# Kernel optimization log

Measured on AMD Instinct MI355X. Metric: run time of the kernel, lower is better.

## Reference

```python
import jax, jax.numpy as jnp
import numpy as np

B, S, D, H, N = 8, 1024, 1024, 16, 16  # batch, seq, hidden, heads, num_ns_tokens
HD = D // H


def setup_inputs() -> dict:
    key = jax.random.key(0)
    ks = jax.random.split(key, 8)
    s = 0.02
    return {
        "x": jax.random.normal(ks[0], (B, S, D), jnp.float32),
        "Wq_shared": jax.random.normal(ks[1], (D, D), jnp.float32) * s,
        "Wk_shared": jax.random.normal(ks[2], (D, D), jnp.float32) * s,
        "Wv_shared": jax.random.normal(ks[3], (D, D), jnp.float32) * s,
        "Wq_ded": jax.random.normal(ks[4], (N, D, D), jnp.float32) * s,
        "Wk_ded": jax.random.normal(ks[5], (N, D, D), jnp.float32) * s,
        "Wv_ded": jax.random.normal(ks[6], (N, D, D), jnp.float32) * s,
        "Wo": jax.random.normal(ks[7], (D, D), jnp.float32) * s,
    }


def reference(x, Wq_shared, Wk_shared, Wv_shared, Wq_ded, Wk_ded, Wv_ded, Wo):
    b, s, d = x.shape
    n = Wq_ded.shape[0]

    def proj(Ws, Wd):
        shared = x @ Ws                                   # [b,s,d]
        ded = jnp.einsum('bnd,ndo->bno', x[:, :n], Wd)    # first n tokens use dedicated weights
        return jnp.concatenate([ded, shared[:, n:]], axis=1)

    q = proj(Wq_shared, Wq_ded).reshape(b, s, H, HD)
    k = proj(Wk_shared, Wk_ded).reshape(b, s, H, HD)
    v = proj(Wv_shared, Wv_ded).reshape(b, s, H, HD)

    scores = jnp.einsum('bqhd,bkhd->bhqk', q, k) / jnp.sqrt(jnp.float32(HD))
    causal = jnp.tril(jnp.ones((s, s), dtype=bool))
    scores = jnp.where(causal, scores, jnp.float32(-1e9))
    attn = jax.nn.softmax(scores, axis=-1)
    out = jnp.einsum('bhqk,bkhd->bqhd', attn, v).reshape(b, s, d)
    output = out @ Wo
    return (output, k, v)
```

## Files before the change

kernel.cpp:

```cpp
#include <hip/hip_runtime.h>
#include <cstdint>


typedef unsigned short u16;
typedef __attribute__((ext_vector_type(8)))  __bf16 bf16x8;
typedef __attribute__((ext_vector_type(8)))  u16    u16x8;
typedef __attribute__((ext_vector_type(4)))  float  f32x4;

#define BSD   (8u * 1024u * 1024u)
#define QSCALE 0.18033688011112042f

__device__ __forceinline__ u16 f2bf(float f) {
    unsigned u = __builtin_bit_cast(unsigned, f);
    u += 0x7fffu + ((u >> 16) & 1u);
    return (u16)(u >> 16);
}

__device__ __forceinline__ unsigned pack_bf2(float p0, float p1) {
    return __builtin_amdgcn_perm(__builtin_bit_cast(unsigned, p1),
                                 __builtin_bit_cast(unsigned, p0), 0x07060302u);
}

__device__ __forceinline__ void gl_lds16(const void* g, void* l) {
    __builtin_amdgcn_global_load_lds(
        (const __attribute__((address_space(1))) unsigned*)g,
        (__attribute__((address_space(3))) unsigned*)l, 16, 0, 0);
}

#define FENCE asm volatile("" ::: "memory")
#define WAITV(n) asm volatile("s_waitcnt vmcnt(" #n ")" ::: "memory")

__global__ __launch_bounds__(256) void cvt_fused(
        const float* __restrict__ Wq, const float* __restrict__ Wk,
        const float* __restrict__ Wv, const float* __restrict__ Wo,
        u16* __restrict__ WTcat, u16* __restrict__ WoT,
        const float4* __restrict__ x, u16* __restrict__ xb) {
    __shared__ float t[32][33];
    int z = blockIdx.z;
    if (z < 4) {
        const float* src = (z == 0) ? Wq : (z == 1) ? Wk : (z == 2) ? Wv : Wo;
        u16* dst = (z < 3) ? (WTcat + (size_t)z * 1024 * 1024) : WoT;
        int k0 = blockIdx.x * 32, n0 = blockIdx.y * 32;
        int xx = threadIdx.x & 31, yy = threadIdx.x >> 5;
#pragma unroll
        for (int i = 0; i < 4; ++i)
            t[yy + 8 * i][xx] = src[(size_t)(k0 + yy + 8 * i) * 1024 + n0 + xx];
        __syncthreads();
#pragma unroll
        for (int i = 0; i < 4; ++i)
            dst[(size_t)(n0 + yy + 8 * i) * 1024 + k0 + xx] = f2bf(t[xx][yy + 8 * i]);
    } else {
        int lb = (z - 4) * 1024 + blockIdx.y * 32 + blockIdx.x;
        int i = lb * 256 + threadIdx.x;
        float4 v = x[i];
        ushort4 o;
        o.x = f2bf(v.x); o.y = f2bf(v.y); o.z = f2bf(v.z); o.w = f2bf(v.w);
        ((ushort4*)xb)[i] = o;
    }
}

__global__ __launch_bounds__(512, 2) void gemm_qkv(
        const u16* __restrict__ A, const u16* __restrict__ Bt,
        float* __restrict__ fout, u16* __restrict__ q_attn,
        u16* __restrict__ k_attn) {
    const int K = 1024, NT = 16;
    __shared__ u16 As[3][128 * 64];
    __shared__ u16 Bs[3][256 * 64];
    int tid = threadIdx.x;
    int w = tid >> 6, lane = tid & 63;
    int m0 = blockIdx.y * 128, n0 = blockIdx.x * 256;
    int wm = w & 1, wn = w >> 1;
    int lr = lane & 15, kg = lane >> 4;

    f32x4 acc[4][4] = {};

    auto stageAll = [&](int buf, int t) {
#pragma unroll
        for (int s = 0; s < 2; ++s) {
            int ci = s * 512 + tid;
            int row = ci >> 3, cg = (ci & 7) ^ (row & 7);
            gl_lds16(A + (size_t)(m0 + row) * K + t * 64 + cg * 8, &As[buf][ci * 8]);
        }
#pragma unroll
        for (int s = 0; s < 4; ++s) {
            int ci = s * 512 + tid;
            int row = ci >> 3, cg = (ci & 7) ^ (row & 7);
            gl_lds16(Bt + (size_t)(n0 + row) * K + t * 64 + cg * 8, &Bs[buf][ci * 8]);
        }
    };

    stageAll(0, 0);
    stageAll(1, 1);
    WAITV(6);
    FENCE; __builtin_amdgcn_s_barrier(); FENCE;

    int cur = 0;
    for (int t = 0; t < NT; ++t) {
        int stb = cur + 2; if (stb >= 3) stb -= 3;
        const u16* Ac = As[cur];
        const u16* Bc = Bs[cur];
        {
            bf16x8 af[4], bf[4];
#pragma unroll
            for (int mi = 0; mi < 4; ++mi) {
                int row = wm * 64 + mi * 16 + lr;
                af[mi] = __builtin_bit_cast(bf16x8,
                    *(const u16x8*)&Ac[row * 64 + ((kg ^ (row & 7)) * 8)]);
            }
#pragma unroll
            for (int ni = 0; ni < 4; ++ni) {
                int row = wn * 64 + ni * 16 + lr;
                bf[ni] = __builtin_bit_cast(bf16x8,
                    *(const u16x8*)&Bc[row * 64 + ((kg ^ (row & 7)) * 8)]);
            }
            if (t + 2 < NT) stageAll(stb, t + 2);
            __builtin_amdgcn_s_setprio(1);
#pragma unroll
            for (int mi = 0; mi < 4; ++mi)
#pragma unroll
                for (int ni = 0; ni < 4; ++ni)
                    acc[mi][ni] = __builtin_amdgcn_mfma_f32_16x16x32_bf16(
                        af[mi], bf[ni], acc[mi][ni], 0, 0, 0);
            __builtin_amdgcn_s_setprio(0);
        }
        {
            bf16x8 af[4], bf[4];
#pragma unroll
            for (int mi = 0; mi < 4; ++mi) {
                int row = wm * 64 + mi * 16 + lr;
                af[mi] = __builtin_bit_cast(bf16x8,
                    *(const u16x8*)&Ac[row * 64 + (((4 + kg) ^ (row & 7)) * 8)]);
            }
#pragma unroll
            for (int ni = 0; ni < 4; ++ni) {
                int row = wn * 64 + ni * 16 + lr;
                bf[ni] = __builtin_bit_cast(bf16x8,
                    *(const u16x8*)&Bc[row * 64 + (((4 + kg) ^ (row & 7)) * 8)]);
            }
            __builtin_amdgcn_s_setprio(1);
#pragma unroll
            for (int mi = 0; mi < 4; ++mi)
#pragma unroll
                for (int ni = 0; ni < 4; ++ni)
                    acc[mi][ni] = __builtin_amdgcn_mfma_f32_16x16x32_bf16(
                        af[mi], bf[ni], acc[mi][ni], 0, 0, 0);
            __builtin_amdgcn_s_setprio(0);
        }
        if (t < NT - 1) {
            if (t + 2 < NT) { WAITV(6); }
            else            { WAITV(0); }
            FENCE; __builtin_amdgcn_s_barrier(); FENCE;
        }
        cur = cur + 1; if (cur >= 3) cur -= 3;
    }

    int matId = n0 >> 10;
    int ncol0 = (n0 & 1023) + wn * 64;
#pragma unroll
    for (int am = 0; am < 4; ++am) {
        int mbase = m0 + wm * 64 + am * 16 + kg * 4;
#pragma unroll
        for (int bn = 0; bn < 4; ++bn) {
            int col = ncol0 + bn * 16 + lr;
#pragma unroll
            for (int r = 0; r < 4; ++r) {
                int mm = mbase + r;
                float v = acc[am][bn][r];
                size_t idx = (size_t)mm * 1024 + col;
                if (matId == 0) {
                    q_attn[idx] = f2bf(v * QSCALE);
                } else if (matId == 1) {
                    fout[(size_t)BSD + idx] = v;
                    k_attn[idx] = f2bf(v);
                } else {
                    fout[(size_t)2 * BSD + idx] = v;
                }
            }
        }
    }
}

#define LDfrag(BUF, bufi, row, ks)                                            \
    __builtin_bit_cast(bf16x8, *(const u16x8*)&BUF[bufi]                      \
        [(row) * 64 + ((((ks) * 4 + kg) ^ ((row) & 7)) * 8)])

#define PH(bufi, mh, nh, STAGE_STMT, GATE_STMT) do {                          \
    bf16x8 af_[2][2], bq_[2][2];                                              \
    _Pragma("unroll") for (int mi = 0; mi < 2; ++mi) {                        \
        int arow = wm * 64 + (mh) * 32 + mi * 16 + lr;                        \
        _Pragma("unroll") for (int ks = 0; ks < 2; ++ks)                      \
            af_[mi][ks] = LDfrag(As, bufi, arow, ks);                         \
    }                                                                         \
    _Pragma("unroll") for (int ni = 0; ni < 2; ++ni) {                        \
        int brow = wn * 64 + (nh) * 32 + ni * 16 + lr;                        \
        _Pragma("unroll") for (int ks = 0; ks < 2; ++ks)                      \
            bq_[ni][ks] = LDfrag(Bs, bufi, brow, ks);                         \
    }                                                                         \
    STAGE_STMT;                                                               \
    GATE_STMT;                                                                \
    FENCE; __builtin_amdgcn_s_barrier(); FENCE;                               \
    asm volatile("s_waitcnt lgkmcnt(0)" ::: "memory");                        \
    __builtin_amdgcn_s_setprio(1);                                            \
    _Pragma("unroll") for (int ks = 0; ks < 2; ++ks)                          \
    _Pragma("unroll") for (int mi = 0; mi < 2; ++mi)                          \
    _Pragma("unroll") for (int ni = 0; ni < 2; ++ni)                          \
        acc[(mh) * 2 + mi][(nh) * 2 + ni] =                                   \
            __builtin_amdgcn_mfma_f32_16x16x32_bf16(                          \
                af_[mi][ks], bq_[ni][ks],                                     \
                acc[(mh) * 2 + mi][(nh) * 2 + ni], 0, 0, 0);                  \
    __builtin_amdgcn_s_setprio(0);                                            \
    FENCE; __builtin_amdgcn_s_barrier(); FENCE;                               \
} while (0)

__global__ __launch_bounds__(512, 2) void gemm8p_wo(
        const u16* __restrict__ A, const u16* __restrict__ Bt,
        float* __restrict__ fout) {
    const int K = 1024, nt = 16;
    __shared__ u16 As[2][128 * 64];
    __shared__ u16 Bs[2][256 * 64];
    int tid = threadIdx.x;
    int w = tid >> 6, lane = tid & 63;
    int m0 = blockIdx.y * 128, n0 = blockIdx.x * 256;
    int wm = w & 1, wn = w >> 1;
    int lr = lane & 15, kg = lane >> 4;

    f32x4 acc[4][4] = {};

    auto stageA = [&](int buf, int half, int t) {
        int ci = ((w & 3) << 6) + lane + ((w >> 2) << 9) + (half << 8);
        int row = ci >> 3, cg = (ci & 7) ^ (row & 7);
        gl_lds16(A + (size_t)(m0 + row) * K + t * 64 + cg * 8, &As[buf][ci * 8]);
    };
    auto stageB = [&](int buf, int half, int t) {
#pragma unroll
        for (int j = 0; j < 2; ++j) {
            int u = w + 8 * j;
            int ci = ((u >> 2) << 9) + ((u & 3) << 6) + lane + (half << 8);
            int row = ci >> 3, cg = (ci & 7) ^ (row & 7);
            gl_lds16(Bt + (size_t)(n0 + row) * K + t * 64 + cg * 8, &Bs[buf][ci * 8]);
        }
    };

    stageA(0, 0, 0);
    stageB(0, 0, 0);
    stageA(0, 1, 0);
    stageB(0, 1, 0);
    WAITV(3);
    FENCE; __builtin_amdgcn_s_barrier(); FENCE;

    for (int t = 0; t < nt - 1; ++t) {
        int cur = t & 1, nxt = cur ^ 1;
        PH(cur, 0, 0, stageA(nxt, 0, t + 1), WAITV(3));
        PH(cur, 1, 0, stageB(nxt, 0, t + 1), WAITV(3));
        PH(cur, 1, 1, stageA(nxt, 1, t + 1), ((void)0));
        PH(cur, 0, 1, stageB(nxt, 1, t + 1), WAITV(3));
    }
    PH(1, 0, 0, ((void)0), WAITV(2));
    PH(1, 1, 0, ((void)0), WAITV(0));
    PH(1, 1, 1, ((void)0), ((void)0));
    PH(1, 0, 1, ((void)0), ((void)0));

#pragma unroll
    for (int am = 0; am < 4; ++am) {
        int mbase = m0 + wm * 64 + am * 16 + kg * 4;
#pragma unroll
        for (int bn = 0; bn < 4; ++bn) {
            int col = n0 + wn * 64 + bn * 16 + lr;
#pragma unroll
            for (int r = 0; r < 4; ++r)
                fout[(size_t)(mbase + r) * 1024 + col] = acc[am][bn][r];
        }
    }
}

__global__ __launch_bounds__(512) void ded_partial(
        const float* __restrict__ x, const float* __restrict__ Wq,
        const float* __restrict__ Wk, const float* __restrict__ Wv,
        float* __restrict__ part) {
    int dc = blockIdx.x, n = blockIdx.y, mat = blockIdx.z;
    const float* W = ((mat == 0) ? Wq : (mat == 1) ? Wk : Wv) +
                     (size_t)n * 1024 * 1024;
    __shared__ float xs[8 * 128];
    __shared__ float4 red[8 * 256];
    int tid = threadIdx.x;
    for (int i = tid; i < 1024; i += 512) {
        int b = i >> 7, d = i & 127;
        xs[i] = x[((size_t)b * 1024 + n) * 1024 + dc * 128 + d];
    }
    __syncthreads();
    int h = tid >> 8, c = tid & 255;
    int o0 = c * 4;
    int dbase = dc * 128 + h * 64;
    float4 acc[8];
#pragma unroll
    for (int b = 0; b < 8; ++b) acc[b] = make_float4(0.f, 0.f, 0.f, 0.f);
    for (int d0 = 0; d0 < 64; d0 += 8) {
        float4 w[8];
#pragma unroll
        for (int j = 0; j < 8; ++j)
            w[j] = *(const float4*)&W[(size_t)(dbase + d0 + j) * 1024 + o0];
#pragma unroll
        for (int j = 0; j < 8; ++j) {
#pragma unroll
            for (int b = 0; b < 8; ++b) {
                float xv = xs[b * 128 + h * 64 + d0 + j];
                acc[b].x += xv * w[j].x;
                acc[b].y += xv * w[j].y;
                acc[b].z += xv * w[j].z;
                acc[b].w += xv * w[j].w;
            }
        }
    }
    if (h == 1) {
#pragma unroll
        for (int b = 0; b < 8; ++b) red[b * 256 + c] = acc[b];
    }
    __syncthreads();
    if (h == 0) {
#pragma unroll
        for (int b = 0; b < 8; ++b) {
            float4 r = red[b * 256 + c];
            acc[b].x += r.x; acc[b].y += r.y; acc[b].z += r.z; acc[b].w += r.w;
            *(float4*)&part[(size_t)(((mat * 8 + dc) * 8 + b) * 16 + n) * 1024 + o0] = acc[b];
        }
    }
}

__global__ __launch_bounds__(256) void fix_vt(
        const float* __restrict__ part, float* __restrict__ d_out,
        u16* __restrict__ q_attn, u16* __restrict__ k_attn,
        const float* __restrict__ vf, u16* __restrict__ vT) {
    __shared__ float t[64][65];
    int bid = blockIdx.x;
    int tid = threadIdx.x;

    if (bid < 384) {
        int mat = bid >> 7, b = (bid >> 4) & 7, n = bid & 15;
        int o0 = tid * 4;
        float v[4] = {0.f, 0.f, 0.f, 0.f};
        for (int dc = 0; dc < 8; ++dc) {
            float4 p = *(const float4*)&part[(size_t)(((mat * 8 + dc) * 8 + b) * 16 + n) * 1024 + o0];
            v[0] += p.x; v[1] += p.y; v[2] += p.z; v[3] += p.w;
        }
#pragma unroll
        for (int j = 0; j < 4; ++j) {
            int col = o0 + j;
            size_t idx = ((size_t)b * 1024 + n) * 1024 + col;
            if (mat == 0) {
                q_attn[idx] = f2bf(v[j] * QSCALE);
            } else if (mat == 1) {
                d_out[(size_t)BSD + idx] = v[j];
                k_attn[idx] = f2bf(v[j]);
            } else {
                d_out[(size_t)2 * BSD + idx] = v[j];
                int h = col >> 6, hd = col & 63;
                vT[((size_t)((b * 16 + h) * 64 + hd)) * 1024 + n] = f2bf(v[j]);
            }
        }
        return;
    }

    int id = bid - 384;
    int st = id & 15, h = (id >> 4) & 15, b = id >> 8;
    int cg = tid & 15, sl = tid >> 4;
#pragma unroll
    for (int p = 0; p < 4; ++p) {
        int s = p * 16 + sl;
        float4 v = *(const float4*)&vf[
            ((size_t)(b * 1024 + st * 64 + s)) * 1024 + h * 64 + cg * 4];
        t[cg * 4 + 0][s] = v.x;
        t[cg * 4 + 1][s] = v.y;
        t[cg * 4 + 2][s] = v.z;
        t[cg * 4 + 3][s] = v.w;
    }
    __syncthreads();
    int hd = tid >> 2, sc = (tid & 3) * 16;
    if (st == 0 && sc == 0) return;
    u16* dst = vT + ((size_t)((b * 16 + h) * 64 + hd)) * 1024 + st * 64 + sc;
#pragma unroll
    for (int c = 0; c < 4; ++c) {
        ushort4 o;
        o.x = f2bf(t[hd][sc + c * 4 + 0]);
        o.y = f2bf(t[hd][sc + c * 4 + 1]);
        o.z = f2bf(t[hd][sc + c * 4 + 2]);
        o.w = f2bf(t[hd][sc + c * 4 + 3]);
        *(ushort4*)(dst + c * 4) = o;
    }
}

__global__ __launch_bounds__(256) void attn(
        const u16* __restrict__ q_attn, const u16* __restrict__ k_attn,
        const u16* __restrict__ vT, u16* __restrict__ O) {
    int qt = 7 - blockIdx.x;
    int h = blockIdx.y, b = blockIdx.z;
    const u16* Qg = q_attn + ((size_t)(b * 1024) + qt * 128) * 1024 + h * 64;
    const u16* Kg = k_attn + ((size_t)(b * 1024)) * 1024 + h * 64;
    const u16* Vg = vT + (size_t)((b * 16 + h) * 64) * 1024;

    __shared__ u16 Qs[128 * 64];
    __shared__ u16 Ks[64 * 64];
    __shared__ u16 Vs[64 * 64];
    __shared__ u16 Ps[128 * 64];
    __shared__ float red[4 * 32];

    int tid = threadIdx.x, wave = tid >> 6, lane = tid & 63;
    int lr = lane & 15, kg = lane >> 4;

#pragma unroll
    for (int j = 0; j < 4; ++j) {
        int ci = j * 256 + tid;
        int row = ci >> 3, cg = (ci & 7) ^ (row & 7);
        gl_lds16(Qg + (size_t)row * 1024 + cg * 8, Qs + ci * 8);
    }

    float l_acc[2] = {0.f, 0.f};
    f32x4 oacc[2][4] = {};

    int nkt = 2 * qt + 2;
    for (int kt = 0; kt < nkt; ++kt) {
        __syncthreads();
#pragma unroll
        for (int j = 0; j < 2; ++j) {
            int ci = j * 256 + tid;
            int row = ci >> 3, cg = (ci & 7) ^ (row & 7);
            gl_lds16(Kg + (size_t)(kt * 64 + row) * 1024 + cg * 8, Ks + ci * 8);
            gl_lds16(Vg + (size_t)row * 1024 + kt * 64 + cg * 8, Vs + ci * 8);
        }
        __syncthreads();

        bool wactive = (qt * 128 + wave * 32 + 31) >= kt * 64;
        if (wactive) {
            f32x4 sacc[4][2] = {};
#pragma unroll
            for (int ks = 0; ks < 2; ++ks) {
                bf16x8 af[4], bq[2];
#pragma unroll
                for (int mi = 0; mi < 4; ++mi) {
                    int row = mi * 16 + lr;
                    af[mi] = __builtin_bit_cast(bf16x8,
                        *(const u16x8*)&Ks[row * 64 + (((ks * 4 + kg) ^ (row & 7)) * 8)]);
                }
#pragma unroll
                for (int nj = 0; nj < 2; ++nj) {
                    int qr = wave * 32 + nj * 16 + lr;
                    bq[nj] = __builtin_bit_cast(bf16x8,
                        *(const u16x8*)&Qs[qr * 64 + (((ks * 4 + kg) ^ (qr & 7)) * 8)]);
                }
#pragma unroll
                for (int mi = 0; mi < 4; ++mi)
#pragma unroll
                    for (int nj = 0; nj < 2; ++nj)
                        sacc[mi][nj] = __builtin_amdgcn_mfma_f32_16x16x32_bf16(
                            af[mi], bq[nj], sacc[mi][nj], 0, 0, 0);
            }

            if (kt >= 2 * qt) {
#pragma unroll
                for (int mi = 0; mi < 4; ++mi)
#pragma unroll
                    for (int nj = 0; nj < 2; ++nj)
#pragma unroll
                        for (int r = 0; r < 4; ++r) {
                            int kk_g = kt * 64 + mi * 16 + kg * 4 + r;
                            int q_g  = qt * 128 + wave * 32 + nj * 16 + lr;
                            if (kk_g > q_g) sacc[mi][nj][r] = -1e30f;
                        }
            }

#pragma unroll
            for (int nj = 0; nj < 2; ++nj) {
                int q = wave * 32 + nj * 16 + lr;
                float lsum = 0.f;
#pragma unroll
                for (int mi = 0; mi < 4; ++mi) {
                    float p0 = __builtin_amdgcn_exp2f(sacc[mi][nj][0]);
                    float p1 = __builtin_amdgcn_exp2f(sacc[mi][nj][1]);
                    float p2 = __builtin_amdgcn_exp2f(sacc[mi][nj][2]);
                    float p3 = __builtin_amdgcn_exp2f(sacc[mi][nj][3]);
                    lsum += (p0 + p1) + (p2 + p3);
                    int kkc = mi * 2 + (kg >> 1);
                    int off = q * 64 + ((kkc ^ (q & 7)) * 8) + (kg & 1) * 4;
                    uint2 w2;
                    w2.x = pack_bf2(p0, p1);
                    w2.y = pack_bf2(p2, p3);
                    *(uint2*)&Ps[off] = w2;
                }
                l_acc[nj] += lsum;
            }

#pragma unroll
            for (int ks = 0; ks < 2; ++ks) {
                bf16x8 ap[2], bv[4];
#pragma unroll
                for (int mi = 0; mi < 2; ++mi) {
                    int q = wave * 32 + mi * 16 + lr;
                    ap[mi] = __builtin_bit_cast(bf16x8,
                        *(const u16x8*)&Ps[q * 64 + (((ks * 4 + kg) ^ (q & 7)) * 8)]);
                }
#pragma unroll
                for (int nj = 0; nj < 4; ++nj) {
                    int hd = nj * 16 + lr;
                    bv[nj] = __builtin_bit_cast(bf16x8,
                        *(const u16x8*)&Vs[hd * 64 + (((ks * 4 + kg) ^ (hd & 7)) * 8)]);
                }
#pragma unroll
                for (int mi = 0; mi < 2; ++mi)
#pragma unroll
                    for (int nj = 0; nj < 4; ++nj)
                        oacc[mi][nj] = __builtin_amdgcn_mfma_f32_16x16x32_bf16(
                            ap[mi], bv[nj], oacc[mi][nj], 0, 0, 0);
            }
        }
    }

#pragma unroll
    for (int nj = 0; nj < 2; ++nj) {
        float l = l_acc[nj];
        l += __shfl_xor(l, 16);
        l += __shfl_xor(l, 32);
        if (kg == 0) red[wave * 32 + nj * 16 + lr] = l;
    }
#pragma unroll
    for (int mi = 0; mi < 2; ++mi) {
        f32x4 lv = *(f32x4*)&red[wave * 32 + mi * 16 + kg * 4];
        f32x4 rv;
#pragma unroll
        for (int r = 0; r < 4; ++r) rv[r] = __builtin_amdgcn_rcpf(lv[r]);
#pragma unroll
        for (int nj = 0; nj < 4; ++nj)
#pragma unroll
            for (int r = 0; r < 4; ++r) {
                int q_local = wave * 32 + mi * 16 + kg * 4 + r;
                size_t row = (size_t)b * 1024 + qt * 128 + q_local;
                O[row * 1024 + h * 64 + nj * 16 + lr] =
                    f2bf(oacc[mi][nj][r] * rv[r]);
            }
    }
}

extern "C" void kernel_launch(void* const* d_in, const int* in_sizes, int n_in,
                              void* d_out, int out_size, void* d_ws, size_t ws_size,
                              hipStream_t stream) {
    const float* x   = (const float*)d_in[0];
    const float* Wq  = (const float*)d_in[1];
    const float* Wk  = (const float*)d_in[2];
    const float* Wv  = (const float*)d_in[3];
    const float* Wqd = (const float*)d_in[4];
    const float* Wkd = (const float*)d_in[5];
    const float* Wvd = (const float*)d_in[6];
    const float* Wo  = (const float*)d_in[7];
    float* out = (float*)d_out;

    char* ws = (char*)d_ws;
    u16*   WTcat  = (u16*)(ws);
    u16*   WoT    = (u16*)(ws + 6291456);
    u16*   xb     = (u16*)(ws + 8388608);
    u16*   q_attn = (u16*)(ws + 25165824);
    u16*   k_attn = (u16*)(ws + 41943040);
    u16*   vT     = (u16*)(ws + 58720256);
    u16*   Ow     = (u16*)(ws + 75497472);
    float* part   = (float*)(ws + 92274688);

    cvt_fused<<<dim3(32, 32, 12), 256, 0, stream>>>(
        Wq, Wk, Wv, Wo, WTcat, WoT, (const float4*)x, xb);
    gemm_qkv<<<dim3(12, 64), 512, 0, stream>>>(xb, WTcat, out, q_attn, k_attn);
    ded_partial<<<dim3(8, 16, 3), 512, 0, stream>>>(x, Wqd, Wkd, Wvd, part);
    fix_vt<<<dim3(2432), 256, 0, stream>>>(
        part, out, q_attn, k_attn, out + (size_t)2 * BSD, vT);
    attn<<<dim3(8, 16, 8), 256, 0, stream>>>(q_attn, k_attn, vT, Ow);
    gemm8p_wo<<<dim3(4, 64), 512, 0, stream>>>(Ow, WoT, out);
}
```

Before: 458.1 us.

## Double-buffer K/V tiles in attention and keep Q fragments in registers

The attention kernel now double-buffers the K and V tiles in LDS. It issues the async global-to-LDS load for the next key tile before computing the current one, and needs only one barrier per iteration instead of two. The Q fragments are loaded once directly from global memory into registers, which removes the Q LDS tile and the repeated LDS reads of Q. Separately, ded_partial gets a launch-bounds occupancy hint of 2 and a partial unroll of its inner loop. The changes trade more LDS for the K/V buffers and more register pressure for better overlap of loads with MFMA work.

```diff
diff --git a/kernel.cpp b/kernel.cpp
--- a/kernel.cpp
+++ b/kernel.cpp
@@ -273,7 +273,7 @@
     }
 }
 
-__global__ __launch_bounds__(512) void ded_partial(
+__global__ __launch_bounds__(512, 2) void ded_partial(
         const float* __restrict__ x, const float* __restrict__ Wq,
         const float* __restrict__ Wk, const float* __restrict__ Wv,
         float* __restrict__ part) {
@@ -294,6 +294,7 @@
     float4 acc[8];
 #pragma unroll
     for (int b = 0; b < 8; ++b) acc[b] = make_float4(0.f, 0.f, 0.f, 0.f);
+#pragma unroll 2
     for (int d0 = 0; d0 < 64; d0 += 8) {
         float4 w[8];
 #pragma unroll
@@ -397,61 +398,63 @@
     const u16* Kg = k_attn + ((size_t)(b * 1024)) * 1024 + h * 64;
     const u16* Vg = vT + (size_t)((b * 16 + h) * 64) * 1024;
 
-    __shared__ u16 Qs[128 * 64];
-    __shared__ u16 Ks[64 * 64];
-    __shared__ u16 Vs[64 * 64];
+    __shared__ u16 Ks[2][64 * 64];
+    __shared__ u16 Vs[2][64 * 64];
     __shared__ u16 Ps[128 * 64];
     __shared__ float red[4 * 32];
 
     int tid = threadIdx.x, wave = tid >> 6, lane = tid & 63;
     int lr = lane & 15, kg = lane >> 4;
 
-#pragma unroll
-    for (int j = 0; j < 4; ++j) {
-        int ci = j * 256 + tid;
-        int row = ci >> 3, cg = (ci & 7) ^ (row & 7);
-        gl_lds16(Qg + (size_t)row * 1024 + cg * 8, Qs + ci * 8);
-    }
-
-    float l_acc[2] = {0.f, 0.f};
-    f32x4 oacc[2][4] = {};
-
-    int nkt = 2 * qt + 2;
-    for (int kt = 0; kt < nkt; ++kt) {
-        __syncthreads();
+    bf16x8 bq_reg[2][2];
+#pragma unroll
+    for (int ks = 0; ks < 2; ++ks)
+#pragma unroll
+        for (int nj = 0; nj < 2; ++nj) {
+            int qr = wave * 32 + nj * 16 + lr;
+            bq_reg[ks][nj] = __builtin_bit_cast(bf16x8,
+                *(const u16x8*)(Qg + (size_t)qr * 1024 + (ks * 4 + kg) * 8));
+        }
+
+    auto stageKV = [&](int buf, int kt) {
 #pragma unroll
         for (int j = 0; j < 2; ++j) {
             int ci = j * 256 + tid;
             int row = ci >> 3, cg = (ci & 7) ^ (row & 7);
-            gl_lds16(Kg + (size_t)(kt * 64 + row) * 1024 + cg * 8, Ks + ci * 8);
-            gl_lds16(Vg + (size_t)row * 1024 + kt * 64 + cg * 8, Vs + ci * 8);
-        }
-        __syncthreads();
+            gl_lds16(Kg + (size_t)(kt * 64 + row) * 1024 + cg * 8, &Ks[buf][ci * 8]);
+            gl_lds16(Vg + (size_t)row * 1024 + kt * 64 + cg * 8, &Vs[buf][ci * 8]);
+        }
+    };
+
+    float l_acc[2] = {0.f, 0.f};
+    f32x4 oacc[2][4] = {};
+
+    int nkt = 2 * qt + 2;
+    stageKV(0, 0);
+    __syncthreads();
+
+    for (int kt = 0; kt < nkt; ++kt) {
+        int cur = kt & 1;
+        if (kt + 1 < nkt) stageKV(cur ^ 1, kt + 1);
 
         bool wactive = (qt * 128 + wave * 32 + 31) >= kt * 64;
         if (wactive) {
             f32x4 sacc[4][2] = {};
 #pragma unroll
             for (int ks = 0; ks < 2; ++ks) {
-                bf16x8 af[4], bq[2];
+                bf16x8 af[4];
 #pragma unroll
                 for (int mi = 0; mi < 4; ++mi) {
                     int row = mi * 16 + lr;
                     af[mi] = __builtin_bit_cast(bf16x8,
-                        *(const u16x8*)&Ks[row * 64 + (((ks * 4 + kg) ^ (row & 7)) * 8)]);
-                }
-#pragma unroll
-                for (int nj = 0; nj < 2; ++nj) {
-                    int qr = wave * 32 + nj * 16 + lr;
-                    bq[nj] = __builtin_bit_cast(bf16x8,
-                        *(const u16x8*)&Qs[qr * 64 + (((ks * 4 + kg) ^ (qr & 7)) * 8)]);
+                        *(const u16x8*)&Ks[cur][row * 64 + (((ks * 4 + kg) ^ (row & 7)) * 8)]);
                 }
 #pragma unroll
                 for (int mi = 0; mi < 4; ++mi)
 #pragma unroll
                     for (int nj = 0; nj < 2; ++nj)
                         sacc[mi][nj] = __builtin_amdgcn_mfma_f32_16x16x32_bf16(
-                            af[mi], bq[nj], sacc[mi][nj], 0, 0, 0);
+                            af[mi], bq_reg[ks][nj], sacc[mi][nj], 0, 0, 0);
             }
 
             if (kt >= 2 * qt) {
@@ -501,7 +504,7 @@
                 for (int nj = 0; nj < 4; ++nj) {
                     int hd = nj * 16 + lr;
                     bv[nj] = __builtin_bit_cast(bf16x8,
-                        *(const u16x8*)&Vs[hd * 64 + (((ks * 4 + kg) ^ (hd & 7)) * 8)]);
+                        *(const u16x8*)&Vs[cur][hd * 64 + (((ks * 4 + kg) ^ (hd & 7)) * 8)]);
                 }
 #pragma unroll
                 for (int mi = 0; mi < 2; ++mi)
@@ -511,6 +514,8 @@
                             ap[mi], bv[nj], oacc[mi][nj], 0, 0, 0);
             }
         }
+
+        if (kt + 1 < nkt) __syncthreads();
     }
 
 #pragma unroll
```

New measurement: 461.7 us. Within noise of the previous version (+0.8%).
